# Kernel optimization log

Measured on AMD Instinct MI355X. Metric: run time of the kernel, lower is better.

Reference implementation:

```python
import jax, jax.numpy as jnp
import numpy as np
from jax import lax

B, C_IN, H, W = 128, 3, 64, 64
HID = 128          # encoder hidden channels
D = 256            # embedding_dim
K = 1024           # codebook_size
COMMIT = 0.25      # commitment_cost


def conv(x, w, b, stride=2, pad=1):
    # x: NCHW, w: OIHW (torch Conv2d layout)
    y = lax.conv_general_dilated(x, w, (stride, stride), [(pad, pad), (pad, pad)],
                                 dimension_numbers=('NCHW', 'OIHW', 'NCHW'))
    return y + b[None, :, None, None]


def conv_t(x, w, b, stride=2, pad=1):
    # torch ConvTranspose2d: w is (in, out, kh, kw); equivalent to a conv with
    # lhs dilation = stride, flipped kernel, padding k-1-pad.
    k = w.shape[2]
    w_ = jnp.flip(w, (2, 3)).transpose(1, 0, 2, 3)  # -> (out, in, kh, kw)
    p = k - 1 - pad
    y = lax.conv_general_dilated(x, w_, (1, 1), [(p, p), (p, p)],
                                 lhs_dilation=(stride, stride),
                                 dimension_numbers=('NCHW', 'OIHW', 'NCHW'))
    return y + b[None, :, None, None]


def setup_inputs() -> dict:
    key = jax.random.key(0)
    ks = jax.random.split(key, 10)
    s = 0.05
    return {
        'x':        jax.random.normal(ks[0], (B, C_IN, H, W), jnp.float32),
        'enc_w1':   jax.random.normal(ks[1], (HID, C_IN, 4, 4), jnp.float32) * s,
        'enc_b1':   jnp.zeros((HID,), jnp.float32),
        'enc_w2':   jax.random.normal(ks[2], (D, HID, 4, 4), jnp.float32) * s,
        'enc_b2':   jnp.zeros((D,), jnp.float32),
        'dec_w1':   jax.random.normal(ks[3], (D, HID, 4, 4), jnp.float32) * s,   # ConvT: (in,out,kh,kw)
        'dec_b1':   jnp.zeros((HID,), jnp.float32),
        'dec_w2':   jax.random.normal(ks[4], (HID, C_IN, 4, 4), jnp.float32) * s,
        'dec_b2':   jnp.zeros((C_IN,), jnp.float32),
        'codebook': jax.random.normal(ks[5], (K, D), jnp.float32),  # embedding.weight.normal_()
    }


def vqvae_forward(x, enc_w1, enc_b1, enc_w2, enc_b2,
                  dec_w1, dec_b1, dec_w2, dec_b2, codebook):
    # ----- encoder -----
    h = jax.nn.relu(conv(x, enc_w1, enc_b1))          # (B, HID, 32, 32)
    e = conv(h, enc_w2, enc_b2)                        # (B, D, 16, 16)

    # ----- VectorQuantizerEMA.forward (eval mode, no mask) -----
    inputs = e.transpose(0, 2, 3, 1)                   # BCHW -> BHWC
    in_shape = inputs.shape
    flat = inputs.reshape(-1, D)                       # (N, D), N = B*16*16

    # squared L2 distances to every code: (N, K)
    dist = (jnp.sum(flat * flat, axis=1, keepdims=True)
            + jnp.sum(codebook * codebook, axis=1)
            - 2.0 * flat @ codebook.T)

    # max_one_hot(-distances) with straight-through gradients
    logits = -dist
    idx = jnp.argmax(logits, axis=-1)                  # (N,)
    oh = jax.nn.one_hot(idx, K, dtype=logits.dtype)
    flat_oh = oh + logits - lax.stop_gradient(logits)  # values == one-hot

    n_lat = in_shape[1] * in_shape[2]                  # H*W latents
    oh_encodings = flat_oh.reshape(in_shape[0], n_lat, K).transpose(0, 2, 1)  # (B, K, n)

    # quantize under no_grad (torch.no_grad block)
    quantized = lax.stop_gradient(flat_oh @ codebook).reshape(in_shape)

    e_latent_loss = jnp.mean((quantized - inputs) ** 2)
    loss = COMMIT * e_latent_loss

    # straight-through estimator
    quantized = inputs + lax.stop_gradient(quantized - inputs)

    avg_probs = jnp.mean(flat_oh, axis=0)
    perplexity = jnp.exp(-jnp.sum(avg_probs * jnp.log(avg_probs + 1e-10)))

    quantized_nchw = quantized.transpose(0, 3, 1, 2)   # BHWC -> BCHW

    # ----- decoder -----
    d1 = jax.nn.relu(conv_t(quantized_nchw, dec_w1, dec_b1))  # (B, HID, 32, 32)
    x_hat = conv_t(d1, dec_w2, dec_b2)                        # (B, 3, 64, 64)

    return x_hat, loss, perplexity, oh_encodings


def reference(x, enc_w1, enc_b1, enc_w2, enc_b2,
              dec_w1, dec_b1, dec_w2, dec_b2, codebook):
    return vqvae_forward(x, enc_w1, enc_b1, enc_w2, enc_b2,
                         dec_w1, dec_b1, dec_w2, dec_b2, codebook)
```

## Files before the change

kernel.cpp:

```cpp
#include <hip/hip_runtime.h>
#include <stdint.h>

#define NB   128
#define CIN  3
#define HID  128
#define DEM  256
#define KCB  1024
#define NLAT 32768

typedef __bf16 bf16x8 __attribute__((ext_vector_type(8)));
typedef _Float16 f16x8 __attribute__((ext_vector_type(8)));
typedef float  f32x4  __attribute__((ext_vector_type(4)));

__device__ inline unsigned short f2bf(float f) {
    unsigned u = __builtin_bit_cast(unsigned, f);
    u = (u + 0x7fff + ((u >> 16) & 1)) >> 16;
    return (unsigned short)u;
}

__global__ __launch_bounds__(256) void k_conv1(const float* __restrict__ x,
        const float* __restrict__ w, const float* __restrict__ bias,
        unsigned short* __restrict__ hA) {
    __shared__ float sx[3][66][66];
    const int b = blockIdx.y;
    const int ocg = blockIdx.x;
    const int oc0 = ocg * 16;
    const int tid = threadIdx.x;
    for (int i = tid; i < 3 * 66 * 66; i += 256) ((float*)sx)[i] = 0.f;
    __syncthreads();
    const float* xb = x + (size_t)b * (3 * 64 * 64);
    for (int i = tid; i < 3 * 64 * 64; i += 256) {
        int ic = i >> 12; int rem = i & 4095; int y = rem >> 6; int xx = rem & 63;
        sx[ic][y + 1][xx + 1] = xb[i];
    }
    __syncthreads();
    for (int j = 0; j < 4; ++j) {
        int pos = tid + j * 256;
        int oy = pos >> 5, ox = pos & 31;
        float acc[16];
        #pragma unroll
        for (int i = 0; i < 16; ++i) acc[i] = 0.f;
        int iy0 = 2 * oy;
        int ix0 = 2 * ox;
        for (int ic = 0; ic < 3; ++ic) {
            float p[16];
            #pragma unroll
            for (int ky = 0; ky < 4; ++ky)
                #pragma unroll
                for (int kx = 0; kx < 4; ++kx)
                    p[ky * 4 + kx] = sx[ic][iy0 + ky][ix0 + kx];
            #pragma unroll
            for (int oc = 0; oc < 16; ++oc) {
                const float* wp = w + ((oc0 + oc) * 3 + ic) * 16;
                float a = acc[oc];
                #pragma unroll
                for (int t = 0; t < 16; ++t) a = fmaf(p[t], wp[t], a);
                acc[oc] = a;
            }
        }
        unsigned short rec[32];
        #pragma unroll
        for (int oc = 0; oc < 16; ++oc) {
            float v = acc[oc] + bias[oc0 + oc];
            v = v > 0.f ? v : 0.f;
            _Float16 hh = (_Float16)v;
            float hf = (float)hh;
            _Float16 ll = (_Float16)((v - hf) * 2048.0f);
            rec[oc] = __builtin_bit_cast(unsigned short, hh);
            rec[16 + oc] = __builtin_bit_cast(unsigned short, ll);
        }
        uint4* dst = (uint4*)(hA + ((size_t)(b * 8 + ocg) * 1024 + pos) * 32);
        uint4* r4 = (uint4*)rec;
        dst[0] = r4[0]; dst[1] = r4[1]; dst[2] = r4[2]; dst[3] = r4[3];
    }
}

__global__ void k_packw2f16(const float* __restrict__ w, unsigned short* __restrict__ wp2) {
    int t = blockIdx.x * 256 + threadIdx.x;
    int oc = t >> 7, rest = t & 127;
    int c0 = rest >> 4, ci = rest & 15;
    const float* src = w + ((size_t)(oc * 128 + c0 * 16 + ci)) * 16;
    float tv[16];
    #pragma unroll
    for (int i = 0; i < 16; i += 4) {
        float4 v = *(const float4*)(src + i);
        tv[i] = v.x; tv[i + 1] = v.y; tv[i + 2] = v.z; tv[i + 3] = v.w;
    }
    #pragma unroll
    for (int ks = 0; ks < 8; ++ks) {
        int ky = ks >> 1, kxp = ks & 1;
        #pragma unroll
        for (int kxh = 0; kxh < 2; ++kxh) {
            float v = tv[ky * 4 + 2 * kxp + kxh];
            _Float16 hh = (_Float16)v;
            float hf = (float)hh;
            _Float16 ll = (_Float16)((v - hf) * 2048.0f);
            size_t base = ((size_t)(c0 * 8 + ks) * 256 + oc) * 64 + kxh * 16 + ci;
            wp2[base]      = __builtin_bit_cast(unsigned short, hh);
            wp2[base + 32] = __builtin_bit_cast(unsigned short, ll);
        }
    }
}

__global__ __launch_bounds__(512) void k_conv2_mfma(const unsigned short* __restrict__ hA,
        const unsigned short* __restrict__ wp2, const float* __restrict__ bias,
        float* __restrict__ e) {
    __shared__ __attribute__((aligned(16))) unsigned short As[321 * 40];
    __shared__ __attribute__((aligned(16))) unsigned short Bs[2][128][72];
    const int tid = threadIdx.x;
    const int b = blockIdx.y;
    const int ocg = blockIdx.x >> 2, yq = blockIdx.x & 3;
    const int lane = tid & 63, wv = tid >> 6;
    const int wm = wv >> 2, wn = wv & 3;
    const int lr = lane & 15, hi = lane >> 4;

    if (tid < 40) As[320 * 40 + tid] = 0;

    f32x4 acc0[2][2], acc1[2][2];
    #pragma unroll
    for (int i = 0; i < 2; ++i)
        #pragma unroll
        for (int j = 0; j < 2; ++j) {
            acc0[i][j] = (f32x4){0.f, 0.f, 0.f, 0.f};
            acc1[i][j] = (f32x4){0.f, 0.f, 0.f, 0.f};
        }

    for (int c0 = 0; c0 < 8; ++c0) {
        __syncthreads();
        {
            const size_t cbase = (size_t)(b * 8 + c0) * 1024;
            for (int p = tid; p < 1280; p += 512) {
                int l = p >> 7, rem = p & 127;
                int ix = rem >> 2, q = rem & 3;
                int iy = 8 * yq - 1 + l;
                uint4* dst = (uint4*)(As + (l * 32 + (ix & 1) * 16 + (ix >> 1)) * 40 + q * 8);
                if (iy >= 0 && iy < 32)
                    *dst = *(const uint4*)(hA + (cbase + iy * 32 + ix) * 32 + q * 8);
                else
                    *dst = (uint4){0u, 0u, 0u, 0u};
            }
        }
        {
            const unsigned short* src = wp2 + ((size_t)(c0 * 8 + 0) * 256 + ocg * 128) * 64;
            for (int p = tid; p < 1024; p += 512) {
                int oc = p >> 3, q = p & 7;
                *(uint4*)(&Bs[0][oc][q * 8]) = *(const uint4*)(src + oc * 64 + q * 8);
            }
        }
        __syncthreads();
        for (int ks = 0; ks < 8; ++ks) {
            const int ky = ks >> 1, kxp = ks & 1;
            if (ks < 7) {
                const unsigned short* src = wp2 + ((size_t)(c0 * 8 + ks + 1) * 256 + ocg * 128) * 64;
                const int buf = (ks + 1) & 1;
                for (int p = tid; p < 1024; p += 512) {
                    int oc = p >> 3, q = p & 7;
                    *(uint4*)(&Bs[buf][oc][q * 8]) = *(const uint4*)(src + oc * 64 + q * 8);
                }
            }
            const unsigned short* bsb = &Bs[ks & 1][0][0];
            f16x8 bh[2], bl[2];
            #pragma unroll
            for (int nf = 0; nf < 2; ++nf) {
                const unsigned short* bp = bsb + (wn * 32 + nf * 16 + lr) * 72 + hi * 8;
                bh[nf] = *(const f16x8*)bp;
                bl[nf] = *(const f16x8*)(bp + 32);
            }
            const int o = 2 * kxp - 1 + (hi >> 1);
            const int ix = 2 * lr + o;
            const bool xv = (ix >= 0) && (ix < 32);
            const int sbase = (o & 1) * 16 + (ix >> 1);
            #pragma unroll
            for (int mf = 0; mf < 2; ++mf) {
                int l = 2 * (wm * 2 + mf) + ky;
                int slot = xv ? (l * 32 + sbase) : 320;
                const unsigned short* ap = As + slot * 40 + (hi & 1) * 8;
                f16x8 a0 = *(const f16x8*)ap;
                f16x8 a1 = *(const f16x8*)(ap + 16);
                #pragma unroll
                for (int nf = 0; nf < 2; ++nf) {
                    acc0[mf][nf] = __builtin_amdgcn_mfma_f32_16x16x32_f16(a0, bh[nf], acc0[mf][nf], 0, 0, 0);
                    acc1[mf][nf] = __builtin_amdgcn_mfma_f32_16x16x32_f16(a0, bl[nf], acc1[mf][nf], 0, 0, 0);
                    acc1[mf][nf] = __builtin_amdgcn_mfma_f32_16x16x32_f16(a1, bh[nf], acc1[mf][nf], 0, 0, 0);
                }
            }
            __syncthreads();
        }
    }
    #pragma unroll
    for (int mf = 0; mf < 2; ++mf) {
        int oy = yq * 4 + wm * 2 + mf;
        #pragma unroll
        for (int nf = 0; nf < 2; ++nf) {
            int oc = ocg * 128 + wn * 32 + nf * 16 + lr;
            float bv = bias[oc];
            #pragma unroll
            for (int r = 0; r < 4; ++r) {
                int ox = hi * 4 + r;
                size_t erow = (size_t)b * 256 + (size_t)oy * 16 + ox;
                e[erow * 256 + oc] = acc0[mf][nf][r] + acc1[mf][nf][r] * (1.0f / 2048.0f) + bv;
            }
        }
    }
}

__global__ void k_cnorm(const float* __restrict__ cb, float* __restrict__ cn) {
    int k = blockIdx.x * 256 + threadIdx.x;
    const float* cp = cb + (size_t)k * 256;
    float s = 0.f;
    #pragma unroll 8
    for (int d = 0; d < 256; d += 4) {
        float4 v = *(const float4*)(cp + d);
        s = fmaf(v.x, v.x, s); s = fmaf(v.y, v.y, s);
        s = fmaf(v.z, v.z, s); s = fmaf(v.w, v.w, s);
    }
    cn[k] = s;
}

__global__ void k_packcbp(const float* __restrict__ cb, unsigned short* __restrict__ cbp) {
    int t = blockIdx.x * 256 + threadIdx.x;
    int c = t >> 8, d = t & 255;
    float v = cb[(size_t)c * 256 + d];
    _Float16 hh = (_Float16)v;
    float hf = (float)hh;
    _Float16 ll = (_Float16)((v - hf) * 2048.0f);
    int g = c >> 4, lr = c & 15;
    int kq = d >> 5, rem = d & 31, hi = rem >> 3, el = rem & 7;
    size_t b0 = ((((size_t)(g * 8 + kq) * 2 + 0) * 4 + hi) * 16 + lr) * 8 + el;
    size_t b1 = ((((size_t)(g * 8 + kq) * 2 + 1) * 4 + hi) * 16 + lr) * 8 + el;
    cbp[b0] = __builtin_bit_cast(unsigned short, hh);
    cbp[b1] = __builtin_bit_cast(unsigned short, ll);
}

__global__ __launch_bounds__(512) void k_vq_mfma(const float* __restrict__ e,
        const unsigned short* __restrict__ cbp, const float* __restrict__ cn,
        const float* __restrict__ cb,
        int* __restrict__ idx, int* __restrict__ counts, float* __restrict__ sse,
        float* __restrict__ oh) {
    __shared__ __attribute__((aligned(16))) unsigned short As[64 * 520];
    __shared__ float redS[8][64];
    __shared__ int   redI[8][64];
    __shared__ int   winner[64];
    __shared__ float sred[64];
    const int tid = threadIdx.x;
    const int lane = tid & 63;
    const int wv = tid >> 6;
    const int lr = lane & 15, hi = lane >> 4;
    const int row0 = blockIdx.x * 64;

    {
        int row = tid >> 3, seg = tid & 7;
        const float* src = e + (size_t)(row0 + row) * 256 + seg * 32;
        unsigned short hb[32], lb[32];
        #pragma unroll
        for (int i = 0; i < 32; i += 4) {
            float4 v = *(const float4*)(src + i);
            float vv[4] = {v.x, v.y, v.z, v.w};
            #pragma unroll
            for (int q = 0; q < 4; ++q) {
                _Float16 hh = (_Float16)vv[q];
                float hf = (float)hh;
                _Float16 ll = (_Float16)((vv[q] - hf) * 2048.0f);
                hb[i + q] = __builtin_bit_cast(unsigned short, hh);
                lb[i + q] = __builtin_bit_cast(unsigned short, ll);
            }
        }
        uint4* dh = (uint4*)(As + row * 520 + seg * 32);
        uint4* dl = (uint4*)(As + row * 520 + 256 + seg * 32);
        #pragma unroll
        for (int u = 0; u < 4; ++u) { dh[u] = ((uint4*)hb)[u]; dl[u] = ((uint4*)lb)[u]; }
    }
    __syncthreads();

    float best_s[4][4];
    int   best_i[4][4];
    #pragma unroll
    for (int a = 0; a < 4; ++a)
        #pragma unroll
        for (int r = 0; r < 4; ++r) { best_s[a][r] = 3.4e38f; best_i[a][r] = 0; }

    for (int ncg = 0; ncg < 4; ++ncg) {
        f32x4 acc0[4][2], acc1[4][2];
        #pragma unroll
        for (int i = 0; i < 4; ++i)
            #pragma unroll
            for (int j = 0; j < 2; ++j) {
                acc0[i][j] = (f32x4){0.f, 0.f, 0.f, 0.f};
                acc1[i][j] = (f32x4){0.f, 0.f, 0.f, 0.f};
            }
        const int gbase = ncg * 16 + wv * 2;
        #pragma unroll
        for (int kq = 0; kq < 8; ++kq) {
            f16x8 bh[2], bl[2];
            #pragma unroll
            for (int nf = 0; nf < 2; ++nf) {
                const unsigned short* bp = cbp
                    + (((size_t)((gbase + nf) * 8 + kq) * 2 + 0) * 4 + hi) * 128 + lr * 8;
                bh[nf] = *(const f16x8*)bp;
                bl[nf] = *(const f16x8*)(bp + 512);
            }
            #pragma unroll
            for (int mf = 0; mf < 4; ++mf) {
                const unsigned short* ap = As + (mf * 16 + lr) * 520 + kq * 32 + hi * 8;
                f16x8 a0 = *(const f16x8*)ap;
                f16x8 a1 = *(const f16x8*)(ap + 256);
                #pragma unroll
                for (int nf = 0; nf < 2; ++nf) {
                    acc0[mf][nf] = __builtin_amdgcn_mfma_f32_16x16x32_f16(a0, bh[nf], acc0[mf][nf], 0, 0, 0);
                    acc1[mf][nf] = __builtin_amdgcn_mfma_f32_16x16x32_f16(a0, bl[nf], acc1[mf][nf], 0, 0, 0);
                    acc1[mf][nf] = __builtin_amdgcn_mfma_f32_16x16x32_f16(a1, bh[nf], acc1[mf][nf], 0, 0, 0);
                }
            }
        }
        #pragma unroll
        for (int nf = 0; nf < 2; ++nf) {
            int code = (gbase + nf) * 16 + lr;
            float cnv = cn[code];
            #pragma unroll
            for (int mf = 0; mf < 4; ++mf)
                #pragma unroll
                for (int r = 0; r < 4; ++r) {
                    float dot = fmaf(acc1[mf][nf][r], (1.0f / 2048.0f), acc0[mf][nf][r]);
                    float s = fmaf(-2.0f, dot, cnv);
                    if (s < best_s[mf][r] || (s == best_s[mf][r] && code < best_i[mf][r])) {
                        best_s[mf][r] = s; best_i[mf][r] = code;
                    }
                }
        }
    }
    #pragma unroll
    for (int m = 1; m < 16; m <<= 1) {
        #pragma unroll
        for (int mf = 0; mf < 4; ++mf)
            #pragma unroll
            for (int r = 0; r < 4; ++r) {
                float os = __shfl_xor(best_s[mf][r], m, 64);
                int   oi = __shfl_xor(best_i[mf][r], m, 64);
                if (os < best_s[mf][r] || (os == best_s[mf][r] && oi < best_i[mf][r])) {
                    best_s[mf][r] = os; best_i[mf][r] = oi;
                }
            }
    }
    if (lr == 0) {
        #pragma unroll
        for (int mf = 0; mf < 4; ++mf)
            #pragma unroll
            for (int r = 0; r < 4; ++r) {
                int row = mf * 16 + hi * 4 + r;
                redS[wv][row] = best_s[mf][r];
                redI[wv][row] = best_i[mf][r];
            }
    }
    __syncthreads();
    if (tid < 64) {
        float bs = redS[0][tid]; int bi = redI[0][tid];
        for (int ww = 1; ww < 8; ++ww) {
            float s = redS[ww][tid]; int i2 = redI[ww][tid];
            if (s < bs || (s == bs && i2 < bi)) { bs = s; bi = i2; }
        }
        int rowg = row0 + tid;
        idx[rowg] = bi;
        atomicAdd(counts + bi, 1);
        int bimg = rowg >> 8, n = rowg & 255;
        oh[(size_t)bimg * (KCB * 256) + (size_t)bi * 256 + n] = 1.0f;
        winner[tid] = bi;
    }
    __syncthreads();
    {
        int row = tid >> 3, seg = tid & 7;
        int bi = winner[row];
        const float* cp = cb + (size_t)bi * 256 + seg * 32;
        const float* ep = e + (size_t)(row0 + row) * 256 + seg * 32;
        float s = 0.f;
        #pragma unroll
        for (int i = 0; i < 32; i += 4) {
            float4 a = *(const float4*)(cp + i);
            float4 b = *(const float4*)(ep + i);
            float d0 = a.x - b.x, d1 = a.y - b.y, d2 = a.z - b.z, d3 = a.w - b.w;
            s = fmaf(d0, d0, s); s = fmaf(d1, d1, s);
            s = fmaf(d2, d2, s); s = fmaf(d3, d3, s);
        }
        s += __shfl_down(s, 4, 64);
        s += __shfl_down(s, 2, 64);
        s += __shfl_down(s, 1, 64);
        if ((tid & 7) == 0) sred[row] = s;
    }
    __syncthreads();
    if (tid == 0) {
        float t = 0.f;
        for (int i = 0; i < 64; ++i) t += sred[i];
        atomicAdd(sse, t);
    }
}

__global__ void k_cb2bf(const float* __restrict__ cb, unsigned short* __restrict__ cbb) {
    int t = blockIdx.x * 256 + threadIdx.x;
    float4 v = *(const float4*)(cb + (size_t)t * 4);
    ushort4 o;
    o.x = f2bf(v.x); o.y = f2bf(v.y); o.z = f2bf(v.z); o.w = f2bf(v.w);
    *(ushort4*)(cbb + (size_t)t * 4) = o;
}

__global__ void k_packw(const float* __restrict__ w, unsigned short* __restrict__ wp) {
    int t = blockIdx.x * 256 + threadIdx.x;
    int ci = t >> 7, oc = t & 127;
    const float* src = w + ((size_t)ci * 128 + oc) * 16;
    float tv[16];
    #pragma unroll
    for (int i = 0; i < 16; i += 4) {
        float4 v = *(const float4*)(src + i);
        tv[i] = v.x; tv[i + 1] = v.y; tv[i + 2] = v.z; tv[i + 3] = v.w;
    }
    #pragma unroll
    for (int p = 0; p < 4; ++p) {
        int a = p >> 1, b2 = p & 1;
        #pragma unroll
        for (int tap = 0; tap < 4; ++tap) {
            int dy = tap >> 1, dx = tap & 1;
            float v = tv[((1 - a) + 2 * dy) * 4 + (1 - b2) + 2 * dx];
            wp[((((p * 4 + tap) * 128) + oc) << 8) + ci] = f2bf(v);
        }
    }
}

__global__ __launch_bounds__(512) void k_convt1_mfma(const int* __restrict__ idx,
        const unsigned short* __restrict__ cbb, const unsigned short* __restrict__ wp,
        const float* __restrict__ bias, float* __restrict__ d1) {
    __shared__ unsigned short As[257 * 72];
    __shared__ unsigned short Bs[128 * 72];
    __shared__ int sidx[256];
    const int tid = threadIdx.x;
    const int b  = blockIdx.y;
    const int p  = blockIdx.x;
    const int a  = p >> 1, bb2 = p & 1;
    if (tid < 256) sidx[tid] = idx[b * 256 + tid] * 256;
    if (tid < 72)  As[256 * 72 + tid] = 0;
    const int lane = tid & 63;
    const int w    = tid >> 6;
    const int wm = w >> 2, wn = w & 3;
    const int lr = lane & 15, hi = lane >> 4;
    const int koff = hi * 8;
    f32x4 acc[8][2];
    #pragma unroll
    for (int i = 0; i < 8; ++i)
        #pragma unroll
        for (int j = 0; j < 2; ++j) acc[i][j] = (f32x4){0.f, 0.f, 0.f, 0.f};

    for (int c0 = 0; c0 < 256; c0 += 64) {
        for (int tap = 0; tap < 4; ++tap) {
            __syncthreads();
            if (tap == 0) {
                int row = tid >> 1, half = tid & 1;
                const uint4* src = (const uint4*)(cbb + sidx[row] + c0 + half * 32);
                uint4 v0 = src[0], v1 = src[1], v2 = src[2], v3 = src[3];
                uint4* dst = (uint4*)(As + row * 72 + half * 32);
                dst[0] = v0; dst[1] = v1; dst[2] = v2; dst[3] = v3;
            }
            {
                int oc = tid >> 2, q = tid & 3;
                const uint4* src = (const uint4*)(wp + (((p * 4 + tap) * 128 + oc) << 8) + c0 + q * 16);
                uint4 v0 = src[0], v1 = src[1];
                uint4* dst = (uint4*)(Bs + oc * 72 + q * 16);
                dst[0] = v0; dst[1] = v1;
            }
            __syncthreads();
            const int dy = tap >> 1, dx = tap & 1;
            const int xo = lr + bb2 - dx;
            const bool xv = (xo >= 0) && (xo < 16);
            #pragma unroll
            for (int kk = 0; kk < 2; ++kk) {
                bf16x8 aF[8];
                #pragma unroll
                for (int i = 0; i < 8; ++i) {
                    int typ = wm * 8 + i + a - dy;
                    int row = (xv && typ >= 0 && typ < 16) ? typ * 16 + xo : 256;
                    aF[i] = *(const bf16x8*)(As + row * 72 + kk * 32 + koff);
                }
                #pragma unroll
                for (int j = 0; j < 2; ++j) {
                    bf16x8 bF = *(const bf16x8*)(Bs + ((wn * 2 + j) * 16 + lr) * 72 + kk * 32 + koff);
                    #pragma unroll
                    for (int i = 0; i < 8; ++i)
                        acc[i][j] = __builtin_amdgcn_mfma_f32_16x16x32_bf16(aF[i], bF, acc[i][j], 0, 0, 0);
                }
            }
        }
    }
    #pragma unroll
    for (int j = 0; j < 2; ++j) {
        int oc = (wn * 2 + j) * 16 + lr;
        float bv = bias[oc];
        #pragma unroll
        for (int i = 0; i < 8; ++i) {
            int mt = wm * 8 + i;
            int oy = 2 * mt + a;
            float* dp = d1 + (((size_t)b * 128 + oc) * 32 + oy) * 32 + bb2;
            #pragma unroll
            for (int r = 0; r < 4; ++r) {
                float v = acc[i][j][r] + bv;
                v = v > 0.f ? v : 0.f;
                dp[2 * (hi * 4 + r)] = v;
            }
        }
    }
}

__global__ __launch_bounds__(256) void k_convt2(const float* __restrict__ d1,
        const float* __restrict__ w, const float* __restrict__ bias,
        float* __restrict__ xhat) {
    __shared__ float sd[4][34][34];
    const int b = blockIdx.y;
    const int par = blockIdx.x;
    const int a = par >> 1, bb = par & 1;
    const int tid = threadIdx.x;
    const int ky0 = 1 - a, kx0 = 1 - bb;
    float acc[4][3];
    #pragma unroll
    for (int j = 0; j < 4; ++j)
        #pragma unroll
        for (int o = 0; o < 3; ++o) acc[j][o] = 0.f;
    for (int i = tid; i < 4 * 34 * 34; i += 256) ((float*)sd)[i] = 0.f;
    const float* db = d1 + (size_t)b * (128 * 1024);
    for (int c0 = 0; c0 < 128; c0 += 4) {
        __syncthreads();
        for (int i = tid; i < 4096; i += 256) {
            int ci = i >> 10, rem = i & 1023, y = rem >> 5, xx = rem & 31;
            sd[ci][y + 1][xx + 1] = db[(c0 + ci) * 1024 + rem];
        }
        __syncthreads();
        #pragma unroll
        for (int j = 0; j < 4; ++j) {
            int pos = tid + j * 256;
            int my = pos >> 5, mx = pos & 31;
            int iy0 = my + a, ix0 = mx + bb;
            #pragma unroll
            for (int ci = 0; ci < 4; ++ci) {
                float q00 = sd[ci][iy0 + 1][ix0 + 1];
                float q01 = sd[ci][iy0 + 1][ix0];
                float q10 = sd[ci][iy0][ix0 + 1];
                float q11 = sd[ci][iy0][ix0];
                const float* wp = w + (size_t)(c0 + ci) * 3 * 16;
                #pragma unroll
                for (int o = 0; o < 3; ++o) {
                    const float* wq = wp + o * 16;
                    float aa = acc[j][o];
                    aa = fmaf(q00, wq[ky0 * 4 + kx0], aa);
                    aa = fmaf(q01, wq[ky0 * 4 + kx0 + 2], aa);
                    aa = fmaf(q10, wq[(ky0 + 2) * 4 + kx0], aa);
                    aa = fmaf(q11, wq[(ky0 + 2) * 4 + kx0 + 2], aa);
                    acc[j][o] = aa;
                }
            }
        }
    }
    #pragma unroll
    for (int j = 0; j < 4; ++j) {
        int pos = tid + j * 256;
        int my = pos >> 5, mx = pos & 31;
        int oy = 2 * my + a, ox = 2 * mx + bb;
        #pragma unroll
        for (int o = 0; o < 3; ++o)
            xhat[((size_t)b * 3 + o) * 4096 + oy * 64 + ox] = acc[j][o] + bias[o];
    }
}

__global__ void k_final(const int* __restrict__ counts, const float* __restrict__ sse,
                        float* __restrict__ out_loss, float* __restrict__ out_perp) {
    __shared__ float red[256];
    int tid = threadIdx.x;
    float s = 0.f;
    for (int k = tid; k < 1024; k += 256) {
        float p = (float)counts[k] * (1.f / 32768.f);
        s += p * logf(p + 1e-10f);
    }
    red[tid] = s;
    __syncthreads();
    for (int st = 128; st > 0; st >>= 1) {
        if (tid < st) red[tid] += red[tid + st];
        __syncthreads();
    }
    if (tid == 0) {
        *out_perp = expf(-red[0]);
        *out_loss = 0.25f * (*sse) / 8388608.0f;
    }
}

extern "C" void kernel_launch(void* const* d_in, const int* in_sizes, int n_in,
                              void* d_out, int out_size, void* d_ws, size_t ws_size,
                              hipStream_t stream) {
    const float* x   = (const float*)d_in[0];
    const float* ew1 = (const float*)d_in[1];
    const float* eb1 = (const float*)d_in[2];
    const float* ew2 = (const float*)d_in[3];
    const float* eb2 = (const float*)d_in[4];
    const float* dw1 = (const float*)d_in[5];
    const float* db1 = (const float*)d_in[6];
    const float* dw2 = (const float*)d_in[7];
    const float* db2 = (const float*)d_in[8];
    const float* cb  = (const float*)d_in[9];

    float* out  = (float*)d_out;
    float* xhat = out;
    float* loss = out + 1572864;
    float* perp = out + 1572865;
    float* oh   = out + 1572866;

    char* ws = (char*)d_ws;
    unsigned short* hA = (unsigned short*)ws;
    float* e      = (float*)(ws + (size_t)64 * 1024 * 1024);
    int*   idx    = (int*)(ws + (size_t)96 * 1024 * 1024);
    int*   counts = idx + NLAT;
    float* sse    = (float*)(counts + KCB);
    float* cn     = sse + 1;
    unsigned short* cbp = (unsigned short*)ws;
    float* d1     = (float*)ws;
    unsigned short* cbb = (unsigned short*)e;
    unsigned short* wpk = (unsigned short*)(ws + (size_t)65 * 1024 * 1024);
    unsigned short* wp2 = (unsigned short*)(((uintptr_t)oh + 15) & ~(uintptr_t)15);

    hipMemsetAsync(oh, 0, (size_t)33554432 * 4, stream);
    hipMemsetAsync(counts, 0, KCB * 4 + 4, stream);

    k_cnorm<<<4, 256, 0, stream>>>(cb, cn);
    k_packw2f16<<<128, 256, 0, stream>>>(ew2, wp2);
    k_conv1<<<dim3(8, 128), 256, 0, stream>>>(x, ew1, eb1, hA);
    k_conv2_mfma<<<dim3(8, 128), 512, 0, stream>>>(hA, wp2, eb2, e);
    hipMemsetAsync(oh, 0, 2 * 1024 * 1024 + 64, stream);
    k_packcbp<<<1024, 256, 0, stream>>>(cb, cbp);
    k_vq_mfma<<<512, 512, 0, stream>>>(e, cbp, cn, cb, idx, counts, sse, oh);
    k_cb2bf<<<256, 256, 0, stream>>>(cb, cbb);
    k_packw<<<128, 256, 0, stream>>>(dw1, wpk);
    k_convt1_mfma<<<dim3(4, 128), 512, 0, stream>>>(idx, cbb, wpk, db1, d1);
    k_convt2<<<dim3(4, 128), 256, 0, stream>>>(d1, dw2, db2, xhat);
    k_final<<<1, 256, 0, stream>>>(counts, sse, loss, perp);
}
```

Baseline: 697.9 us.

## Load conv2 weights directly in MFMA fragment layout and double rows per block

The packed conv2 weight buffer is reorganised so each lane can read its f16 hi/lo B fragments straight from global memory, which removes the shared-memory B double buffer and the per-ks barriers. Each block now covers 8 output rows instead of 4, so the grid halves and every staged input tile and weight fragment feeds twice as many MFMAs. The cost is more accumulator registers, a larger LDS A tile, and weight reads that go through cache instead of shared memory.

```diff
diff --git a/kernel.cpp b/kernel.cpp
--- a/kernel.cpp
+++ b/kernel.cpp
@@ -75,7 +75,7 @@
     }
 }
 
-__global__ void k_packw2f16(const float* __restrict__ w, unsigned short* __restrict__ wp2) {
+__global__ void k_packwf(const float* __restrict__ w, unsigned short* __restrict__ wpf) {
     int t = blockIdx.x * 256 + threadIdx.x;
     int oc = t >> 7, rest = t & 127;
     int c0 = rest >> 4, ci = rest & 15;
@@ -86,6 +86,7 @@
         float4 v = *(const float4*)(src + i);
         tv[i] = v.x; tv[i + 1] = v.y; tv[i + 2] = v.z; tv[i + 3] = v.w;
     }
+    int g = oc >> 4, lr = oc & 15;
     #pragma unroll
     for (int ks = 0; ks < 8; ++ks) {
         int ky = ks >> 1, kxp = ks & 1;
@@ -95,30 +96,31 @@
             _Float16 hh = (_Float16)v;
             float hf = (float)hh;
             _Float16 ll = (_Float16)((v - hf) * 2048.0f);
-            size_t base = ((size_t)(c0 * 8 + ks) * 256 + oc) * 64 + kxh * 16 + ci;
-            wp2[base]      = __builtin_bit_cast(unsigned short, hh);
-            wp2[base + 32] = __builtin_bit_cast(unsigned short, ll);
+            int d = kxh * 16 + ci;
+            int hi = d >> 3, el = d & 7;
+            size_t base = ((((size_t)(c0 * 8 + ks) * 16 + g) * 2 + 0) * 4 + hi) * 128 + lr * 8 + el;
+            wpf[base]       = __builtin_bit_cast(unsigned short, hh);
+            wpf[base + 512] = __builtin_bit_cast(unsigned short, ll);
         }
     }
 }
 
 __global__ __launch_bounds__(512) void k_conv2_mfma(const unsigned short* __restrict__ hA,
-        const unsigned short* __restrict__ wp2, const float* __restrict__ bias,
+        const unsigned short* __restrict__ wpf, const float* __restrict__ bias,
         float* __restrict__ e) {
-    __shared__ __attribute__((aligned(16))) unsigned short As[321 * 40];
-    __shared__ __attribute__((aligned(16))) unsigned short Bs[2][128][72];
+    __shared__ __attribute__((aligned(16))) unsigned short As[577 * 40];
     const int tid = threadIdx.x;
     const int b = blockIdx.y;
-    const int ocg = blockIdx.x >> 2, yq = blockIdx.x & 3;
+    const int ocg = blockIdx.x >> 1, yh = blockIdx.x & 1;
     const int lane = tid & 63, wv = tid >> 6;
     const int wm = wv >> 2, wn = wv & 3;
     const int lr = lane & 15, hi = lane >> 4;
 
-    if (tid < 40) As[320 * 40 + tid] = 0;
-
-    f32x4 acc0[2][2], acc1[2][2];
-    #pragma unroll
-    for (int i = 0; i < 2; ++i)
+    if (tid < 40) As[576 * 40 + tid] = 0;
+
+    f32x4 acc0[4][2], acc1[4][2];
+    #pragma unroll
+    for (int i = 0; i < 4; ++i)
         #pragma unroll
         for (int j = 0; j < 2; ++j) {
             acc0[i][j] = (f32x4){0.f, 0.f, 0.f, 0.f};
@@ -129,51 +131,37 @@
         __syncthreads();
         {
             const size_t cbase = (size_t)(b * 8 + c0) * 1024;
-            for (int p = tid; p < 1280; p += 512) {
+            for (int p = tid; p < 2304; p += 512) {
                 int l = p >> 7, rem = p & 127;
-                int ix = rem >> 2, q = rem & 3;
-                int iy = 8 * yq - 1 + l;
-                uint4* dst = (uint4*)(As + (l * 32 + (ix & 1) * 16 + (ix >> 1)) * 40 + q * 8);
+                int ixs = rem >> 2, q = rem & 3;
+                int iy = yh * 16 - 1 + l;
+                uint4* dst = (uint4*)(As + (l * 32 + (ixs & 1) * 16 + (ixs >> 1)) * 40 + q * 8);
                 if (iy >= 0 && iy < 32)
-                    *dst = *(const uint4*)(hA + (cbase + iy * 32 + ix) * 32 + q * 8);
+                    *dst = *(const uint4*)(hA + (cbase + iy * 32 + ixs) * 32 + q * 8);
                 else
                     *dst = (uint4){0u, 0u, 0u, 0u};
             }
         }
-        {
-            const unsigned short* src = wp2 + ((size_t)(c0 * 8 + 0) * 256 + ocg * 128) * 64;
-            for (int p = tid; p < 1024; p += 512) {
-                int oc = p >> 3, q = p & 7;
-                *(uint4*)(&Bs[0][oc][q * 8]) = *(const uint4*)(src + oc * 64 + q * 8);
-            }
-        }
         __syncthreads();
+        #pragma unroll
         for (int ks = 0; ks < 8; ++ks) {
             const int ky = ks >> 1, kxp = ks & 1;
-            if (ks < 7) {
-                const unsigned short* src = wp2 + ((size_t)(c0 * 8 + ks + 1) * 256 + ocg * 128) * 64;
-                const int buf = (ks + 1) & 1;
-                for (int p = tid; p < 1024; p += 512) {
-                    int oc = p >> 3, q = p & 7;
-                    *(uint4*)(&Bs[buf][oc][q * 8]) = *(const uint4*)(src + oc * 64 + q * 8);
-                }
-            }
-            const unsigned short* bsb = &Bs[ks & 1][0][0];
             f16x8 bh[2], bl[2];
             #pragma unroll
             for (int nf = 0; nf < 2; ++nf) {
-                const unsigned short* bp = bsb + (wn * 32 + nf * 16 + lr) * 72 + hi * 8;
+                const unsigned short* bp = wpf
+                    + ((((size_t)(c0 * 8 + ks) * 16 + (ocg * 8 + wn * 2 + nf)) * 2 + 0) * 4 + hi) * 128 + lr * 8;
                 bh[nf] = *(const f16x8*)bp;
-                bl[nf] = *(const f16x8*)(bp + 32);
+                bl[nf] = *(const f16x8*)(bp + 512);
             }
             const int o = 2 * kxp - 1 + (hi >> 1);
             const int ix = 2 * lr + o;
             const bool xv = (ix >= 0) && (ix < 32);
             const int sbase = (o & 1) * 16 + (ix >> 1);
             #pragma unroll
-            for (int mf = 0; mf < 2; ++mf) {
-                int l = 2 * (wm * 2 + mf) + ky;
-                int slot = xv ? (l * 32 + sbase) : 320;
+            for (int mf = 0; mf < 4; ++mf) {
+                int l = 2 * (wm * 4 + mf) + ky;
+                int slot = xv ? (l * 32 + sbase) : 576;
                 const unsigned short* ap = As + slot * 40 + (hi & 1) * 8;
                 f16x8 a0 = *(const f16x8*)ap;
                 f16x8 a1 = *(const f16x8*)(ap + 16);
@@ -184,12 +172,11 @@
                     acc1[mf][nf] = __builtin_amdgcn_mfma_f32_16x16x32_f16(a1, bh[nf], acc1[mf][nf], 0, 0, 0);
                 }
             }
-            __syncthreads();
-        }
-    }
-    #pragma unroll
-    for (int mf = 0; mf < 2; ++mf) {
-        int oy = yq * 4 + wm * 2 + mf;
+        }
+    }
+    #pragma unroll
+    for (int mf = 0; mf < 4; ++mf) {
+        int oy = yh * 8 + wm * 4 + mf;
         #pragma unroll
         for (int nf = 0; nf < 2; ++nf) {
             int oc = ocg * 128 + wn * 32 + nf * 16 + lr;
@@ -616,15 +603,15 @@
     float* d1     = (float*)ws;
     unsigned short* cbb = (unsigned short*)e;
     unsigned short* wpk = (unsigned short*)(ws + (size_t)65 * 1024 * 1024);
-    unsigned short* wp2 = (unsigned short*)(((uintptr_t)oh + 15) & ~(uintptr_t)15);
+    unsigned short* wpf = (unsigned short*)(((uintptr_t)oh + 15) & ~(uintptr_t)15);
 
     hipMemsetAsync(oh, 0, (size_t)33554432 * 4, stream);
     hipMemsetAsync(counts, 0, KCB * 4 + 4, stream);
 
     k_cnorm<<<4, 256, 0, stream>>>(cb, cn);
-    k_packw2f16<<<128, 256, 0, stream>>>(ew2, wp2);
+    k_packwf<<<128, 256, 0, stream>>>(ew2, wpf);
     k_conv1<<<dim3(8, 128), 256, 0, stream>>>(x, ew1, eb1, hA);
-    k_conv2_mfma<<<dim3(8, 128), 512, 0, stream>>>(hA, wp2, eb2, e);
+    k_conv2_mfma<<<dim3(4, 128), 512, 0, stream>>>(hA, wpf, eb2, e);
     hipMemsetAsync(oh, 0, 2 * 1024 * 1024 + 64, stream);
     k_packcbp<<<1024, 256, 0, stream>>>(cb, cbp);
     k_vq_mfma<<<512, 512, 0, stream>>>(e, cbp, cn, cb, idx, counts, sse, oh);
```

After: 671.4 us. 1.04x faster.
